# Optimization experiments

Measured on AMD Instinct MI355X. Metric: run time of the kernel, lower is better.

Reference implementation:

```python
import jax, jax.numpy as jnp
import numpy as np

S = 8192          # total tokens (8 images x 1024 patches)
DIM = 1280        # hidden_size
H = 16            # num_heads
DH = DIM // H     # head_dim = 80
N_SEG = 8         # number of image segments (equal-length)


def setup_inputs() -> dict:
    key = jax.random.key(0)
    ks = jax.random.split(key, 8)
    hidden_states = jax.random.normal(ks[0], (S, DIM), dtype=jnp.float32)
    ang = jax.random.uniform(ks[1], (S, DH), dtype=jnp.float32) * (2.0 * np.pi)
    cos = jnp.cos(ang)
    sin = jnp.sin(ang)
    cu_seqlens = (jnp.arange(N_SEG + 1, dtype=jnp.int32) * (S // N_SEG))
    qkv_w = jax.random.normal(ks[2], (3 * DIM, DIM), dtype=jnp.float32) * 0.02
    qkv_b = jax.random.normal(ks[3], (3 * DIM,), dtype=jnp.float32) * 0.02
    proj_w = jax.random.normal(ks[4], (DIM, DIM), dtype=jnp.float32) * 0.02
    proj_b = jax.random.normal(ks[5], (DIM,), dtype=jnp.float32) * 0.02
    return {
        "hidden_states": hidden_states,
        "cos": cos,
        "sin": sin,
        "qkv_w": qkv_w,
        "qkv_b": qkv_b,
        "proj_w": proj_w,
        "proj_b": proj_b,
        "cu_seqlens": cu_seqlens,
    }


def _rotate_half(x):
    d = x.shape[-1] // 2
    return jnp.concatenate([-x[..., d:], x[..., :d]], axis=-1)


def reference(hidden_states, cos, sin, qkv_w, qkv_b, proj_w, proj_b, cu_seqlens):
    s, dim = hidden_states.shape
    dh = cos.shape[-1]
    h = dim // dh
    n_seg = cu_seqlens.shape[0] - 1  # static; segments are equal-length
    L = s // n_seg
    scale = dh ** -0.5

    # fused QKV projection: [S, 3, H, DH]
    qkv = (hidden_states @ qkv_w.T + qkv_b).reshape(s, 3, h, dh)
    q, k, v = qkv[:, 0], qkv[:, 1], qkv[:, 2]

    # RoPE (fp32, broadcast cos/sin over heads)
    cos_b = cos[:, None, :].astype(jnp.float32)
    sin_b = sin[:, None, :].astype(jnp.float32)
    qf, kf = q.astype(jnp.float32), k.astype(jnp.float32)
    q = (qf * cos_b + _rotate_half(qf) * sin_b).astype(q.dtype)
    k = (kf * cos_b + _rotate_half(kf) * sin_b).astype(k.dtype)

    # per-segment (block-diagonal) attention: reshape to [n_seg, L, H, DH]
    qs = q.reshape(n_seg, L, h, dh)
    ks = k.reshape(n_seg, L, h, dh)
    vs = v.reshape(n_seg, L, h, dh)
    scores = jnp.einsum("glhd,gmhd->ghlm", qs, ks) * scale
    attn = jax.nn.softmax(scores, axis=-1)
    out = jnp.einsum("ghlm,gmhd->glhd", attn, vs).reshape(s, dim)
    return out @ proj_w.T + proj_b
```

## Files before the change

### kernel.cpp

```cpp
#include <hip/hip_runtime.h>
#include <hip/hip_bf16.h>
#include <stdint.h>

typedef unsigned short u16;
typedef unsigned int u32;
typedef __attribute__((ext_vector_type(8))) short short8;
typedef __attribute__((ext_vector_type(4))) float f32x4;

#define DEV __device__ __forceinline__

constexpr int S = 8192;
constexpr int DIM = 1280;
constexpr int H = 16;
constexpr int DH = 80;
constexpr int LSEG = 1024;
constexpr int QKVN = 3 * DIM;
constexpr float SCALE = 0.11180339887498949f * 1.4426950408889634f;

DEV u16 f2bf(float f) {
  u32 u = __float_as_uint(f);
  return (u16)((u + 0x7FFFu + ((u >> 16) & 1u)) >> 16);
}
DEV float bf2f(u16 h) { return __uint_as_float(((u32)h) << 16); }
DEV u32 pkbf(float a, float b) {
  __hip_bfloat162 t = __float22bfloat162_rn(float2{a, b});
  u32 r; __builtin_memcpy(&r, &t, 4); return r;
}

DEV void glds16(const void* g, void* l) {
  __builtin_amdgcn_global_load_lds((__attribute__((address_space(1))) void*)g,
                                   (__attribute__((address_space(3))) void*)l,
                                   16, 0, 0);
}
DEV f32x4 mfma16(short8 a, short8 b, f32x4 c) {
  return __builtin_amdgcn_mfma_f32_16x16x32_bf16(a, b, c, 0, 0, 0);
}

__global__ __launch_bounds__(256) void cvt_kernel(
    const float* __restrict__ X, const float* __restrict__ Wq,
    const float* __restrict__ Wp, u16* __restrict__ Xb,
    u16* __restrict__ Wqb, u16* __restrict__ Wpb) {
  size_t i = ((size_t)blockIdx.x * 256 + threadIdx.x) * 4;
  const size_t n1 = (size_t)S * DIM;
  const size_t n2 = (size_t)QKVN * DIM;
  const size_t n3 = (size_t)DIM * DIM;
  const float* src; u16* dst; size_t off;
  if (i < n1)                { src = X;  dst = Xb;  off = i; }
  else if (i < n1 + n2)      { src = Wq; dst = Wqb; off = i - n1; }
  else if (i < n1 + n2 + n3) { src = Wp; dst = Wpb; off = i - n1 - n2; }
  else return;
  float4 v = *(const float4*)(src + off);
  ushort4 r;
  r.x = f2bf(v.x); r.y = f2bf(v.y); r.z = f2bf(v.z); r.w = f2bf(v.w);
  *(ushort4*)(dst + off) = r;
}

__global__ __launch_bounds__(256) void rope_kernel(
    const u16* __restrict__ QKV, const float* __restrict__ cosp,
    const float* __restrict__ sinp, u16* __restrict__ Qp, u16* __restrict__ Kp) {
  int idx = blockIdx.x * 256 + threadIdx.x;
  int c = idx % 5;
  int sh = idx / 5;
  int s = sh >> 4, h = sh & 15;
  const size_t gbase = (size_t)s * QKVN + h * DH + c * 8;
  const size_t pbase = (size_t)sh * 96 + c * 8;
  short8 q0 = *(const short8*)&QKV[gbase];
  short8 q1 = *(const short8*)&QKV[gbase + 40];
  short8 k0 = *(const short8*)&QKV[gbase + DIM];
  short8 k1 = *(const short8*)&QKV[gbase + DIM + 40];
  float4 ca0 = *(const float4*)&cosp[s * DH + c * 8];
  float4 ca1 = *(const float4*)&cosp[s * DH + c * 8 + 4];
  float4 cb0 = *(const float4*)&cosp[s * DH + c * 8 + 40];
  float4 cb1 = *(const float4*)&cosp[s * DH + c * 8 + 44];
  float4 sa0 = *(const float4*)&sinp[s * DH + c * 8];
  float4 sa1 = *(const float4*)&sinp[s * DH + c * 8 + 4];
  float4 sb0 = *(const float4*)&sinp[s * DH + c * 8 + 40];
  float4 sb1 = *(const float4*)&sinp[s * DH + c * 8 + 44];
  float ca[8] = {ca0.x, ca0.y, ca0.z, ca0.w, ca1.x, ca1.y, ca1.z, ca1.w};
  float cb[8] = {cb0.x, cb0.y, cb0.z, cb0.w, cb1.x, cb1.y, cb1.z, cb1.w};
  float sa[8] = {sa0.x, sa0.y, sa0.z, sa0.w, sa1.x, sa1.y, sa1.z, sa1.w};
  float sb[8] = {sb0.x, sb0.y, sb0.z, sb0.w, sb1.x, sb1.y, sb1.z, sb1.w};
  short8 qo0, qo1, ko0, ko1;
#pragma unroll
  for (int j = 0; j < 8; j++) {
    float qa = bf2f((u16)q0[j]), qb = bf2f((u16)q1[j]);
    float ka = bf2f((u16)k0[j]), kb = bf2f((u16)k1[j]);
    qo0[j] = (short)f2bf((qa * ca[j] - qb * sa[j]) * SCALE);
    qo1[j] = (short)f2bf((qb * cb[j] + qa * sb[j]) * SCALE);
    ko0[j] = (short)f2bf(ka * ca[j] - kb * sa[j]);
    ko1[j] = (short)f2bf(kb * cb[j] + ka * sb[j]);
  }
  *(short8*)&Qp[pbase]      = qo0;
  *(short8*)&Qp[pbase + 40] = qo1;
  *(short8*)&Kp[pbase]      = ko0;
  *(short8*)&Kp[pbase + 40] = ko1;
  if (c == 0) {
    short8 z = {};
    *(short8*)&Qp[pbase + 80] = z; *(short8*)&Qp[pbase + 88] = z;
    *(short8*)&Kp[pbase + 80] = z; *(short8*)&Kp[pbase + 88] = z;
  }
}

__global__ __launch_bounds__(256) void vtrans_kernel(
    const u16* __restrict__ QKV, u16* __restrict__ Vt) {
  __shared__ u16 Ls[64 * 88];
  const int s0 = blockIdx.x * 64, h = blockIdx.y;
  const int tid = threadIdx.x;
  for (int cc = tid; cc < 640; cc += 256) {
    int row = cc / 10, c = cc % 10;
    short8 v = *(const short8*)&QKV[(size_t)(s0 + row) * QKVN + 2 * DIM + h * 80 + c * 8];
    *(short8*)&Ls[row * 88 + c * 8] = v;
  }
  __syncthreads();
  for (int cc = tid; cc < 640; cc += 256) {
    int d = cc / 8, sc = cc % 8;
    u16 tmp[8];
#pragma unroll
    for (int j = 0; j < 8; j++) {
      int op = sc * 8 + j;
      int key = ((op & 3) << 4) + (op >> 2);
      tmp[j] = Ls[key * 88 + d];
    }
    *(short8*)&Vt[(size_t)(h * 80 + d) * S + s0 + sc * 8] = *(short8*)tmp;
  }
}

template <bool OUT_F32>
__global__ __launch_bounds__(256, 2) void gemm_bt(
    const u16* __restrict__ A, const u16* __restrict__ B,
    const float* __restrict__ bias, void* __restrict__ C, int K, int N) {
  __shared__ u16 As[2][128 * 32];
  __shared__ u16 Bs[2][128 * 32];
  const int bid = blockIdx.x;
  const int xcd = bid & 7, j = bid >> 3;
  const int m0 = (xcd * 8 + (j & 7)) * 128;
  const int n0 = (j >> 3) * 128;
  const int tid = threadIdx.x;
  const int w = tid >> 6, lane = tid & 63;
  const int quad = lane >> 4, l16 = lane & 15;
  const int wr = (w >> 1) * 64, wc = (w & 1) * 64;
  const int lrow = lane >> 2;
  const int lcol = ((lane & 3) ^ (lrow & 3)) * 8;
  const u16* ga[4]; const u16* gb[4]; u16* la[4]; u16* lb[4];
#pragma unroll
  for (int i = 0; i < 4; i++) {
    int jj = w + 4 * i;
    int s = jj >> 3, c = jj & 7;
    ga[i] = A + (size_t)(m0 + c * 16 + lrow) * K + s * 32 + lcol;
    la[i] = &As[s][c * 512];
    gb[i] = B + (size_t)(n0 + c * 16 + lrow) * K + s * 32 + lcol;
    lb[i] = &Bs[s][c * 512];
  }
  const int fco = (quad ^ (l16 & 3)) * 8;
  f32x4 acc[4][4] = {};
  for (int k0 = 0; k0 < K; k0 += 64) {
    __syncthreads();
#pragma unroll
    for (int i = 0; i < 4; i++) { glds16(ga[i], la[i]); ga[i] += 64; }
#pragma unroll
    for (int i = 0; i < 4; i++) { glds16(gb[i], lb[i]); gb[i] += 64; }
    __syncthreads();
#pragma unroll
    for (int s = 0; s < 2; s++) {
      short8 af[4], bf[4];
#pragma unroll
      for (int i = 0; i < 4; i++)
        af[i] = *(const short8*)&As[s][(wr + i * 16 + l16) * 32 + fco];
#pragma unroll
      for (int i = 0; i < 4; i++)
        bf[i] = *(const short8*)&Bs[s][(wc + i * 16 + l16) * 32 + fco];
#pragma unroll
      for (int i = 0; i < 4; i++)
#pragma unroll
        for (int jj = 0; jj < 4; jj++)
          acc[i][jj] = mfma16(af[i], bf[jj], acc[i][jj]);
    }
  }
#pragma unroll
  for (int jj = 0; jj < 4; jj++) {
    int col = n0 + wc + jj * 16 + l16;
    float bv = bias[col];
#pragma unroll
    for (int i = 0; i < 4; i++) {
#pragma unroll
      for (int r = 0; r < 4; r++) {
        int row = m0 + wr + i * 16 + quad * 4 + r;
        float v = acc[i][jj][r] + bv;
        if (OUT_F32) ((float*)C)[(size_t)row * N + col] = v;
        else         ((u16*)C)[(size_t)row * N + col] = f2bf(v);
      }
    }
  }
}

__global__ __launch_bounds__(256, 2) void attn_kernel(
    const u16* __restrict__ Qp, const u16* __restrict__ Kp,
    const u16* __restrict__ Vt, u16* __restrict__ O) {
  __shared__ u16 Ks[2][64 * 104];
  __shared__ u16 Vs[2][86 * 72];
  __shared__ u16 Ps[4][16 * 72];
  const int bid = blockIdx.x;
  const int phi = bid & 7, qt = (bid >> 3) & 7, pj = bid >> 6;
  const int p = pj * 8 + phi;
  const int g = p >> 4, h = p & 15;
  const int tid = threadIdx.x;
  const int w = tid >> 6, lane = tid & 63;
  const int quad = lane >> 4, l16 = lane & 15;

  short8 aq[2][3];
  const size_t qbase = ((size_t)(g * LSEG + qt * 128 + w * 32 + l16)) * 1536 + h * 96;
#pragma unroll
  for (int mt = 0; mt < 2; mt++)
#pragma unroll
    for (int ks = 0; ks < 3; ks++)
      aq[mt][ks] = *(const short8*)&Qp[qbase + (size_t)mt * 16 * 1536 + ks * 32 + quad * 8];

  const u16* gp[7]; u16* lp0[7]; u16* lp1[7]; int stp[7]; bool act[7];
#pragma unroll
  for (int i = 0; i < 7; i++) {
    int c = w + 4 * i;
    act[i] = (c < 25);
    int cc = act[i] ? c : 0;
    if (cc < 13) {
      int idx = cc * 64 + lane;
      int key = idx / 13, rc = idx % 13;
      int col = rc * 8; if (col >= 96) col = 0;
      gp[i] = Kp + (size_t)(g * LSEG + key) * 1536 + h * 96 + col;
      stp[i] = 64 * 1536;
      lp0[i] = &Ks[0][cc * 512]; lp1[i] = &Ks[1][cc * 512];
    } else {
      int cv = cc - 13;
      int idx = cv * 64 + lane;
      int d = idx / 9, rc = idx % 9;
      int col = rc * 8; if (col >= 64) col = 0;
      if (d >= 80) d = 0;
      gp[i] = Vt + (size_t)(h * 80 + d) * S + g * LSEG + col;
      stp[i] = 64;
      lp0[i] = &Vs[0][cv * 512]; lp1[i] = &Vs[1][cv * 512];
    }
  }
#pragma unroll
  for (int i = 0; i < 7; i++)
    if (act[i]) { glds16(gp[i], lp0[i]); gp[i] += stp[i]; }

  f32x4 o[2][5] = {};
  float lr[2][4] = {};
  u16* psw = &Ps[w][0];

  for (int kb = 0; kb < LSEG / 64; kb++) {
    const int b = kb & 1;
    __syncthreads();
    if (kb < LSEG / 64 - 1) {
      if (b == 0) {
#pragma unroll
        for (int i = 0; i < 7; i++)
          if (act[i]) { glds16(gp[i], lp1[i]); gp[i] += stp[i]; }
      } else {
#pragma unroll
        for (int i = 0; i < 7; i++)
          if (act[i]) { glds16(gp[i], lp0[i]); gp[i] += stp[i]; }
      }
    }
    f32x4 s[2][4] = {};
#pragma unroll
    for (int ks = 0; ks < 3; ks++) {
      short8 bk[4];
#pragma unroll
      for (int nt = 0; nt < 4; nt++)
        bk[nt] = *(const short8*)&Ks[b][(nt * 16 + l16) * 104 + ks * 32 + quad * 8];
#pragma unroll
      for (int mt = 0; mt < 2; mt++)
#pragma unroll
        for (int nt = 0; nt < 4; nt++)
          s[mt][nt] = mfma16(aq[mt][ks], bk[nt], s[mt][nt]);
    }
    short8 vb[5][2];
#pragma unroll
    for (int t = 0; t < 5; t++)
#pragma unroll
      for (int u = 0; u < 2; u++)
        vb[t][u] = *(const short8*)&Vs[b][(t * 16 + l16) * 72 + u * 32 + quad * 8];
#pragma unroll
    for (int mt = 0; mt < 2; mt++) {
#pragma unroll
      for (int r = 0; r < 4; r++) {
        float p0 = __builtin_amdgcn_exp2f(s[mt][0][r]);
        float p1 = __builtin_amdgcn_exp2f(s[mt][1][r]);
        float p2 = __builtin_amdgcn_exp2f(s[mt][2][r]);
        float p3 = __builtin_amdgcn_exp2f(s[mt][3][r]);
        lr[mt][r] += (p0 + p1) + (p2 + p3);
        int row = quad * 4 + r;
        uint2 pk; pk.x = pkbf(p0, p1); pk.y = pkbf(p2, p3);
        *(uint2*)&psw[row * 72 + l16 * 4] = pk;
      }
      short8 pa0 = *(const short8*)&psw[l16 * 72 + quad * 8];
      short8 pa1 = *(const short8*)&psw[l16 * 72 + 32 + quad * 8];
#pragma unroll
      for (int t = 0; t < 5; t++)
        o[mt][t] = mfma16(pa0, vb[t][0], o[mt][t]);
#pragma unroll
      for (int t = 0; t < 5; t++)
        o[mt][t] = mfma16(pa1, vb[t][1], o[mt][t]);
    }
  }
#pragma unroll
  for (int mt = 0; mt < 2; mt++)
#pragma unroll
    for (int r = 0; r < 4; r++) {
      float t = lr[mt][r];
#pragma unroll
      for (int off = 8; off >= 1; off >>= 1) t += __shfl_xor(t, off, 16);
      float inv = 1.f / t;
      int srow = g * LSEG + qt * 128 + w * 32 + mt * 16 + quad * 4 + r;
#pragma unroll
      for (int tt = 0; tt < 5; tt++)
        O[(size_t)srow * DIM + h * DH + tt * 16 + l16] = f2bf(o[mt][tt][r] * inv);
    }
}

extern "C" void kernel_launch(void* const* d_in, const int* in_sizes, int n_in,
                              void* d_out, int out_size, void* d_ws, size_t ws_size,
                              hipStream_t stream) {
  const float* X     = (const float*)d_in[0];
  const float* cosp  = (const float*)d_in[1];
  const float* sinp  = (const float*)d_in[2];
  const float* qkvw  = (const float*)d_in[3];
  const float* qkvb  = (const float*)d_in[4];
  const float* projw = (const float*)d_in[5];
  const float* projb = (const float*)d_in[6];
  float* out = (float*)d_out;

  u16* Xb   = (u16*)d_ws;
  u16* Wqb  = Xb   + (size_t)S * DIM;
  u16* Wpb  = Wqb  + (size_t)QKVN * DIM;
  u16* QKVb = Wpb  + (size_t)DIM * DIM;
  u16* Kp   = QKVb + (size_t)S * QKVN;
  u16* Vt   = Kp   + (size_t)S * H * 96;
  u16* Qp   = Xb;
  u16* AOb  = QKVb;

  cvt_kernel<<<16640, 256, 0, stream>>>(X, qkvw, projw, Xb, Wqb, Wpb);
  gemm_bt<false><<<30 * 64, 256, 0, stream>>>(Xb, Wqb, qkvb, QKVb, DIM, QKVN);
  rope_kernel<<<(S * H * 5) / 256, 256, 0, stream>>>(QKVb, cosp, sinp, Qp, Kp);
  vtrans_kernel<<<dim3(S / 64, H), 256, 0, stream>>>(QKVb, Vt);
  attn_kernel<<<1024, 256, 0, stream>>>(Qp, Kp, Vt, AOb);
  gemm_bt<true><<<10 * 64, 256, 0, stream>>>(AOb, Wpb, projb, out, DIM, DIM);
}
```

Baseline: 340.3 us.

## Rewrite GEMM as 256x256 tile, 8-wave, software-pipelined kernel with setprio

The bf16 GEMM moves from 128x128 tiles with 4 waves and a simple load-then-compute loop to 256x256 tiles with 8 waves. Each tile is split into halves that are prefetched one stage ahead, and MFMA phases are interleaved with global-to-LDS loads using explicit barriers, vmcnt waits and s_setprio. It also remaps blocks across XCDs and uses an XOR swizzle for the 64-wide LDS rows. The aim is more data reuse per tile and hiding load latency behind MFMA work. The cost is a large LDS footprint (128KB per block) and fewer blocks, which hurts tail balance, especially for the 1280x1280 projection, where only 160 blocks are launched.

```diff
diff --git a/kernel.cpp b/kernel.cpp
--- a/kernel.cpp
+++ b/kernel.cpp
@@ -126,66 +126,131 @@
 }
 
 template <bool OUT_F32>
-__global__ __launch_bounds__(256, 2) void gemm_bt(
+__global__ __launch_bounds__(512, 2) void gemm_bt(
     const u16* __restrict__ A, const u16* __restrict__ B,
     const float* __restrict__ bias, void* __restrict__ C, int K, int N) {
-  __shared__ u16 As[2][128 * 32];
-  __shared__ u16 Bs[2][128 * 32];
-  const int bid = blockIdx.x;
-  const int xcd = bid & 7, j = bid >> 3;
-  const int m0 = (xcd * 8 + (j & 7)) * 128;
-  const int n0 = (j >> 3) * 128;
+  __shared__ u16 As[2][2][8192];
+  __shared__ u16 Bs[2][2][8192];
+  const int ntn = N >> 8;
+  const int q = gridDim.x >> 3;
+  const int widx = (blockIdx.x & 7) * q + (blockIdx.x >> 3);
+  const int m0 = (widx / ntn) << 8;
+  const int n0 = (widx % ntn) << 8;
   const int tid = threadIdx.x;
   const int w = tid >> 6, lane = tid & 63;
   const int quad = lane >> 4, l16 = lane & 15;
-  const int wr = (w >> 1) * 64, wc = (w & 1) * 64;
-  const int lrow = lane >> 2;
-  const int lcol = ((lane & 3) ^ (lrow & 3)) * 8;
-  const u16* ga[4]; const u16* gb[4]; u16* la[4]; u16* lb[4];
-#pragma unroll
-  for (int i = 0; i < 4; i++) {
-    int jj = w + 4 * i;
-    int s = jj >> 3, c = jj & 7;
-    ga[i] = A + (size_t)(m0 + c * 16 + lrow) * K + s * 32 + lcol;
-    la[i] = &As[s][c * 512];
-    gb[i] = B + (size_t)(n0 + c * 16 + lrow) * K + s * 32 + lcol;
-    lb[i] = &Bs[s][c * 512];
-  }
-  const int fco = (quad ^ (l16 & 3)) * 8;
-  f32x4 acc[4][4] = {};
-  for (int k0 = 0; k0 < K; k0 += 64) {
-    __syncthreads();
-#pragma unroll
-    for (int i = 0; i < 4; i++) { glds16(ga[i], la[i]); ga[i] += 64; }
-#pragma unroll
-    for (int i = 0; i < 4; i++) { glds16(gb[i], lb[i]); gb[i] += 64; }
-    __syncthreads();
-#pragma unroll
-    for (int s = 0; s < 2; s++) {
-      short8 af[4], bf[4];
+  const int wm = w >> 2, wn = w & 3;
+
+  const int rowoff = w * 8 + (lane >> 3);
+  const int coloff = ((lane & 7) ^ (lane >> 3)) * 8;
+  const u16* pa0 = A + (size_t)(m0 + rowoff) * K + coloff;
+  const u16* pa1 = A + (size_t)(m0 + 128 + rowoff) * K + coloff;
+  const u16* pb0 = B + (size_t)(n0 + rowoff) * K + coloff;
+  const u16* pb1 = B + (size_t)(n0 + 128 + rowoff) * K + coloff;
+  const size_t j64 = (size_t)64 * K;
+
+#define STG(P, DST, kk) do { \
+    glds16((P) + (kk), &(DST)[w * 512]); \
+    glds16((P) + j64 + (kk), &(DST)[4096 + w * 512]); } while (0)
+
+  const int aro = (wm * 16 + l16) * 64;
+  const int bro = (wn * 16 + l16) * 64;
+  const int kc0 = ((quad) ^ (l16 & 7)) * 8;
+  const int kc1 = ((4 + quad) ^ (l16 & 7)) * 8;
+
+  f32x4 acc[8][4] = {};
+  short8 af[4][2], bf0[2][2], bf1[2][2];
+  const int NT = K >> 6;
+
+  STG(pa0, As[0][0], 0); STG(pb0, Bs[0][0], 0);
+  STG(pa1, As[0][1], 0); STG(pb1, Bs[0][1], 0);
+  STG(pa0, As[1][0], 64); STG(pb0, Bs[1][0], 64);
+  asm volatile("s_waitcnt vmcnt(4)" ::: "memory");
+  asm volatile("s_barrier" ::: "memory");
+
+  for (int t = 0; t < NT; ++t) {
+    const int b = t & 1;
+    const int kk1 = (t + 1) << 6, kk2 = (t + 2) << 6;
+#pragma unroll
+    for (int i = 0; i < 4; i++) {
+      af[i][0] = *(const short8*)&As[b][0][aro + i * 2048 + kc0];
+      af[i][1] = *(const short8*)&As[b][0][aro + i * 2048 + kc1];
+    }
+#pragma unroll
+    for (int jj = 0; jj < 2; jj++) {
+      bf0[jj][0] = *(const short8*)&Bs[b][0][bro + jj * 4096 + kc0];
+      bf0[jj][1] = *(const short8*)&Bs[b][0][bro + jj * 4096 + kc1];
+    }
+    if (t + 1 < NT) { STG(pa1, As[b ^ 1][1], kk1); STG(pb1, Bs[b ^ 1][1], kk1); }
+    asm volatile("s_barrier" ::: "memory");
+    __builtin_amdgcn_s_setprio(1);
+#pragma unroll
+    for (int ks = 0; ks < 2; ks++)
 #pragma unroll
       for (int i = 0; i < 4; i++)
-        af[i] = *(const short8*)&As[s][(wr + i * 16 + l16) * 32 + fco];
+#pragma unroll
+        for (int jj = 0; jj < 2; jj++)
+          acc[i][jj] = mfma16(af[i][ks], bf0[jj][ks], acc[i][jj]);
+    __builtin_amdgcn_s_setprio(0);
+    asm volatile("s_barrier" ::: "memory");
+#pragma unroll
+    for (int jj = 0; jj < 2; jj++) {
+      bf1[jj][0] = *(const short8*)&Bs[b][1][bro + jj * 4096 + kc0];
+      bf1[jj][1] = *(const short8*)&Bs[b][1][bro + jj * 4096 + kc1];
+    }
+    if (t + 2 < NT) STG(pa0, As[b][0], kk2);
+    asm volatile("s_barrier" ::: "memory");
+    __builtin_amdgcn_s_setprio(1);
+#pragma unroll
+    for (int ks = 0; ks < 2; ks++)
 #pragma unroll
       for (int i = 0; i < 4; i++)
-        bf[i] = *(const short8*)&Bs[s][(wc + i * 16 + l16) * 32 + fco];
+#pragma unroll
+        for (int jj = 0; jj < 2; jj++)
+          acc[i][2 + jj] = mfma16(af[i][ks], bf1[jj][ks], acc[i][2 + jj]);
+    __builtin_amdgcn_s_setprio(0);
+    asm volatile("s_barrier" ::: "memory");
+#pragma unroll
+    for (int i = 0; i < 4; i++) {
+      af[i][0] = *(const short8*)&As[b][1][aro + i * 2048 + kc0];
+      af[i][1] = *(const short8*)&As[b][1][aro + i * 2048 + kc1];
+    }
+    if (t + 2 < NT) STG(pb0, Bs[b][0], kk2);
+    asm volatile("s_barrier" ::: "memory");
+    __builtin_amdgcn_s_setprio(1);
+#pragma unroll
+    for (int ks = 0; ks < 2; ks++)
 #pragma unroll
       for (int i = 0; i < 4; i++)
 #pragma unroll
-        for (int jj = 0; jj < 4; jj++)
-          acc[i][jj] = mfma16(af[i], bf[jj], acc[i][jj]);
-    }
-  }
-#pragma unroll
-  for (int jj = 0; jj < 4; jj++) {
-    int col = n0 + wc + jj * 16 + l16;
+        for (int jj = 0; jj < 2; jj++)
+          acc[4 + i][jj] = mfma16(af[i][ks], bf0[jj][ks], acc[4 + i][jj]);
+    __builtin_amdgcn_s_setprio(0);
+    asm volatile("s_barrier" ::: "memory");
+    __builtin_amdgcn_s_setprio(1);
+#pragma unroll
+    for (int ks = 0; ks < 2; ks++)
+#pragma unroll
+      for (int i = 0; i < 4; i++)
+#pragma unroll
+        for (int jj = 0; jj < 2; jj++)
+          acc[4 + i][2 + jj] = mfma16(af[i][ks], bf1[jj][ks], acc[4 + i][2 + jj]);
+    __builtin_amdgcn_s_setprio(0);
+    if (t < NT - 2)       asm volatile("s_waitcnt vmcnt(4)" ::: "memory");
+    else if (t == NT - 2) asm volatile("s_waitcnt vmcnt(0)" ::: "memory");
+    asm volatile("s_barrier" ::: "memory");
+  }
+#undef STG
+#pragma unroll
+  for (int nf = 0; nf < 4; nf++) {
+    int col = n0 + nf * 64 + wn * 16 + l16;
     float bv = bias[col];
 #pragma unroll
-    for (int i = 0; i < 4; i++) {
+    for (int mf = 0; mf < 8; mf++) {
 #pragma unroll
       for (int r = 0; r < 4; r++) {
-        int row = m0 + wr + i * 16 + quad * 4 + r;
-        float v = acc[i][jj][r] + bv;
+        int row = m0 + mf * 32 + wm * 16 + quad * 4 + r;
+        float v = acc[mf][nf][r] + bv;
         if (OUT_F32) ((float*)C)[(size_t)row * N + col] = v;
         else         ((u16*)C)[(size_t)row * N + col] = f2bf(v);
       }
@@ -340,9 +405,9 @@
   u16* AOb  = QKVb;
 
   cvt_kernel<<<16640, 256, 0, stream>>>(X, qkvw, projw, Xb, Wqb, Wpb);
-  gemm_bt<false><<<30 * 64, 256, 0, stream>>>(Xb, Wqb, qkvb, QKVb, DIM, QKVN);
+  gemm_bt<false><<<(S / 256) * (QKVN / 256), 512, 0, stream>>>(Xb, Wqb, qkvb, QKVb, DIM, QKVN);
   rope_kernel<<<(S * H * 5) / 256, 256, 0, stream>>>(QKVb, cosp, sinp, Qp, Kp);
   vtrans_kernel<<<dim3(S / 64, H), 256, 0, stream>>>(QKVb, Vt);
   attn_kernel<<<1024, 256, 0, stream>>>(Qp, Kp, Vt, AOb);
-  gemm_bt<true><<<10 * 64, 256, 0, stream>>>(AOb, Wpb, projb, out, DIM, DIM);
-}
+  gemm_bt<true><<<(S / 256) * (DIM / 256), 512, 0, stream>>>(AOb, Wpb, projb, out, DIM, DIM);
+}
```

Measured after the change: 332.7 us. 1.02x faster.
